# Kernel optimization log

Measured on AMD Instinct MI355X. Metric: run time of the kernel, lower is better.

Reference implementation:

```python
import jax, jax.numpy as jnp
import numpy as np

DIM = 240; NH = 6; HD = 20          # dim, num_heads, head_dim = dim // (2*num_heads)
WS = 16; BWS = 8                    # window size, base window size
R = (WS // BWS) ** 2                # spatial_linear in_features (=4)
LW = WS * WS; LB = BWS * BWS

# static relative-position index for a WSxWS window (same construction as torch buffer)
_coords = np.stack(np.meshgrid(np.arange(WS), np.arange(WS), indexing='ij')).reshape(2, -1)
_rel = (_coords[:, :, None] - _coords[:, None, :]).transpose(1, 2, 0).astype(np.int64)
_rel[..., 0] += WS - 1; _rel[..., 1] += WS - 1; _rel[..., 0] *= 2 * WS - 1
RPI = jnp.asarray(_rel.sum(-1))     # [LW, LW]


def conv2d(x, w, b, pad):
    y = jax.lax.conv_general_dilated(x, w, (1, 1), [(pad, pad), (pad, pad)],
                                     dimension_numbers=('NCHW', 'OIHW', 'NCHW'))
    return y + b[None, :, None, None]


def lrelu(x):
    return jnp.where(x >= 0, x, 0.2 * x)  # LeakyReLU(0.2)


def layer_norm(x, g, b, eps=1e-5):
    m = x.mean(-1, keepdims=True)
    v = jnp.mean((x - m) ** 2, axis=-1, keepdims=True)
    return (x - m) * jax.lax.rsqrt(v + eps) * g + b


def setup_inputs() -> dict:
    key = jax.random.key(0)
    ks = iter(jax.random.split(key, 40))
    rn = lambda shape: jax.random.normal(next(ks), shape, jnp.float32) * 0.02
    B, H, W = 2, 256, 256
    pd = (DIM // 4) // 4  # DynamicPosBias pos_dim = 15
    return {
        'x': jax.random.normal(next(ks), (B, H * W, DIM), jnp.float32),
        # DFE (qv projection)
        'c1_w': rn((DIM // 5, DIM, 1, 1)), 'c1_b': jnp.zeros((DIM // 5,), jnp.float32),
        'c2_w': rn((DIM // 5, DIM // 5, 3, 3)), 'c2_b': jnp.zeros((DIM // 5,), jnp.float32),
        'c3_w': rn((DIM, DIM // 5, 1, 1)), 'c3_b': jnp.zeros((DIM,), jnp.float32),
        'lin_w': rn((DIM, DIM, 1, 1)), 'lin_b': jnp.zeros((DIM,), jnp.float32),
        # spatial linear projection Linear(R, 1)
        'sl_w': rn((1, R)), 'sl_b': jnp.zeros((1,), jnp.float32),
        # DynamicPosBias MLP (residual=False)
        'pp_w': rn((pd, 2)), 'pp_b': jnp.zeros((pd,), jnp.float32),
        'ln1_g': jnp.ones((pd,), jnp.float32), 'ln1_b': jnp.zeros((pd,), jnp.float32),
        'p1_w': rn((pd, pd)), 'p1_b': jnp.zeros((pd,), jnp.float32),
        'ln2_g': jnp.ones((pd,), jnp.float32), 'ln2_b': jnp.zeros((pd,), jnp.float32),
        'p2_w': rn((pd, pd)), 'p2_b': jnp.zeros((pd,), jnp.float32),
        'ln3_g': jnp.ones((pd,), jnp.float32), 'ln3_b': jnp.zeros((pd,), jnp.float32),
        'p3_w': rn((NH, pd)), 'p3_b': jnp.zeros((NH,), jnp.float32),
        # output projection
        'proj_w': rn((DIM, DIM)), 'proj_b': jnp.zeros((DIM,), jnp.float32),
        'H': 256, 'W': 256,
    }


def reference(x, c1_w, c1_b, c2_w, c2_b, c3_w, c3_b, lin_w, lin_b, sl_w, sl_b,
              pp_w, pp_b, ln1_g, ln1_b, p1_w, p1_b, ln2_g, ln2_b, p2_w, p2_b,
              ln3_g, ln3_b, p3_w, p3_b, proj_w, proj_b, H, W):
    B, L, C = x.shape
    # ---- DFE feature projection (conv-gated) ----
    xi = jnp.transpose(x, (0, 2, 1)).reshape(B, C, H, W)
    conv = conv2d(lrelu(conv2d(lrelu(conv2d(xi, c1_w, c1_b, 0)), c2_w, c2_b, 1)), c3_w, c3_b, 0)
    qv = conv * conv2d(xi, lin_w, lin_b, 0)                       # [B,C,H,W]
    qv = jnp.transpose(qv, (0, 2, 3, 1))                          # [B,H,W,C]
    # ---- window partition ----
    nh_w, nw_w = H // WS, W // WS
    qv = qv.reshape(B, nh_w, WS, nw_w, WS, C).transpose(0, 1, 3, 2, 4, 5).reshape(-1, LW, C)
    B_ = qv.shape[0]
    qv = qv.reshape(B_, LW, 2, NH, HD).transpose(2, 0, 3, 1, 4)   # [2,B_,NH,LW,HD]
    q, v = qv[0], qv[1]
    # ---- spatial self-correlation ----
    # spatial linear projection of v: [B_,NH,LW,HD] -> [B_,NH,LB,HD]
    vs = v.reshape(B_, NH, BWS, WS // BWS, BWS, WS // BWS, HD)
    vs = vs.transpose(0, 1, 2, 4, 6, 3, 5).reshape(B_, NH, LB, HD, R)
    vs = jnp.einsum('bnkcr,or->bnkc', vs, sl_w) + sl_b            # Linear(R,1), squeezed
    corr = jnp.einsum('bnlc,bnkc->bnlk', q, vs) / HD              # [B_,NH,LW,LB]
    # dynamic relative position bias (MLP over the mother set of relative coords)
    ph = jnp.arange(1 - WS, WS)
    biases = jnp.stack(jnp.meshgrid(ph, ph, indexing='ij')).reshape(2, -1).T.astype(x.dtype)
    pos = biases @ pp_w.T + pp_b
    pos = jax.nn.relu(layer_norm(pos, ln1_g, ln1_b)) @ p1_w.T + p1_b
    pos = jax.nn.relu(layer_norm(pos, ln2_g, ln2_b)) @ p2_w.T + p2_b
    pos = jax.nn.relu(layer_norm(pos, ln3_g, ln3_b)) @ p3_w.T + p3_b  # [(2*WS-1)^2, NH]
    rpb = jnp.take(pos, RPI.reshape(-1), axis=0).reshape(LW, LW, NH).transpose(2, 0, 1)
    # pool key axis to base-window resolution (consistent with spatial_linear_projection grouping)
    rpb = rpb.reshape(NH, LW, BWS, WS // BWS, BWS, WS // BWS).mean((3, 5)).reshape(NH, LW, LB)
    corr = corr + rpb[None]
    x_s = jnp.einsum('bnlk,bnkc->bnlc', corr, vs)
    x_s = x_s.transpose(0, 2, 1, 3).reshape(B_, LW, NH * HD)      # [B_,LW,C/2]
    # ---- channel self-correlation (single-head over merged channels) ----
    qc = q.transpose(0, 2, 1, 3).reshape(B_, LW, NH * HD)
    vc = v.transpose(0, 2, 1, 3).reshape(B_, LW, NH * HD)
    corr_c = jnp.einsum('blc,bld->bcd', qc, vc) / LW              # [B_,C/2,C/2]
    x_c = jnp.einsum('bcd,bld->blc', corr_c, vc)                  # [B_,LW,C/2]
    # ---- window reverse + spatial-channel fusion ----
    def wrev(t):
        return t.reshape(B, nh_w, nw_w, WS, WS, -1).transpose(0, 1, 3, 2, 4, 5).reshape(B, H, W, -1)
    out = jnp.concatenate([wrev(x_s), wrev(x_c)], axis=-1)        # [B,H,W,C]
    out = out @ proj_w.T + proj_b
    return out.reshape(B, L, C)
```

## Files before the change

### kernel.cpp

```cpp
#include <hip/hip_runtime.h>
#include <math.h>

#define NPIX 131072

typedef __attribute__((ext_vector_type(8))) short bfrag;
typedef __attribute__((ext_vector_type(4))) float facc;
typedef __attribute__((ext_vector_type(4))) unsigned short us4;

__device__ __forceinline__ float lrelu_f(float x) { return x >= 0.f ? x : 0.2f * x; }

__device__ __forceinline__ int pix_of(int w, int l) {
    int b = w >> 8, wi = (w >> 4) & 15, wj = w & 15;
    return ((((b << 4) + wi) * 16 + (l >> 4)) << 8) + (wj << 4) + (l & 15);
}

__device__ __forceinline__ unsigned short bf16rn(float f) {
    unsigned u = __builtin_bit_cast(unsigned, f);
    u += 0x7FFFu + ((u >> 16) & 1u);
    return (unsigned short)(u >> 16);
}
__device__ __forceinline__ float bf16tof(unsigned short h) {
    unsigned u = ((unsigned)h) << 16;
    return __builtin_bit_cast(float, u);
}

__device__ __forceinline__ void split_x_body(const float* __restrict__ x,
                                             unsigned short* __restrict__ xs2, int idx)
{
    int row = idx >> 5;
    int k = (idx & 31) * 8;
    float v[8];
    if (k < 240) {
        float4 a = *(const float4*)(x + (size_t)row * 240 + k);
        float4 b = *(const float4*)(x + (size_t)row * 240 + k + 4);
        v[0] = a.x; v[1] = a.y; v[2] = a.z; v[3] = a.w;
        v[4] = b.x; v[5] = b.y; v[6] = b.z; v[7] = b.w;
    } else {
#pragma unroll
        for (int e = 0; e < 8; ++e) v[e] = 0.f;
    }
    bfrag hi, lo;
#pragma unroll
    for (int e = 0; e < 8; ++e) {
        unsigned short h = bf16rn(v[e]);
        hi[e] = (short)h;
        lo[e] = (short)bf16rn(v[e] - bf16tof(h));
    }
    unsigned short* dst = xs2 + (size_t)row * 512 + k;
    *(bfrag*)(dst) = hi;
    *(bfrag*)(dst + 256) = lo;
}

__device__ __forceinline__ void pack_w_body(const float* __restrict__ src,
                                            int rows, int K,
                                            unsigned short* __restrict__ dst,
                                            int total8, int KPAD, int idx)
{
    if (idx >= total8) return;
    int kper = KPAD >> 3;
    int row = idx / kper;
    int k = (idx - row * kper) * 8;
    float v[8];
#pragma unroll
    for (int e = 0; e < 8; ++e) {
        int kk = k + e;
        v[e] = (row < rows && kk < K) ? src[(size_t)row * K + kk] : 0.f;
    }
    bfrag hi, lo;
#pragma unroll
    for (int e = 0; e < 8; ++e) {
        unsigned short h = bf16rn(v[e]);
        hi[e] = (short)h;
        lo[e] = (short)bf16rn(v[e] - bf16tof(h));
    }
    unsigned short* d = dst + (size_t)row * 2 * KPAD + k;
    *(bfrag*)(d) = hi;
    *(bfrag*)(d + KPAD) = lo;
}

__device__ __forceinline__ void pack_c2w_body(const float* __restrict__ c2_w,
                                              unsigned short* __restrict__ c2w2, int idx)
{
    if (idx >= 6912) return;
    int rowid = idx >> 4;
    int c = idx & 15;
    int tap = rowid / 48, n = rowid - tap * 48;
    int ty = tap / 3, tx = tap - ty * 3;
    int lohalf = c >> 3;
    int cbase = (c & 7) * 8;
    bfrag outv;
#pragma unroll
    for (int e = 0; e < 8; ++e) {
        int ci = cbase + e;
        float v = (ci < 48) ? c2_w[(((size_t)n * 48 + ci) * 3 + ty) * 3 + tx] : 0.f;
        unsigned short h = bf16rn(v);
        outv[e] = (short)(lohalf ? bf16rn(v - bf16tof(h)) : h);
    }
    *(bfrag*)(c2w2 + (size_t)rowid * 128 + c * 8) = outv;
}

__global__ __launch_bounds__(256) void pack_all_kernel(
    const float* __restrict__ lin_w, const float* __restrict__ proj_w,
    const float* __restrict__ c3_w, const float* __restrict__ c1_w,
    const float* __restrict__ c2_w, const float* __restrict__ x,
    unsigned short* __restrict__ lin_w2, unsigned short* __restrict__ proj_w2,
    unsigned short* __restrict__ c3_w2, unsigned short* __restrict__ c1_w2,
    unsigned short* __restrict__ c2w2, unsigned short* __restrict__ xs2)
{
    int blk = blockIdx.x, tid = threadIdx.x;
    if (blk < 32)       pack_w_body(lin_w, 240, 240, lin_w2, 8192, 256, blk * 256 + tid);
    else if (blk < 64)  pack_w_body(proj_w, 240, 240, proj_w2, 8192, 256, (blk - 32) * 256 + tid);
    else if (blk < 72)  pack_w_body(c3_w, 240, 48, c3_w2, 2048, 64, (blk - 64) * 256 + tid);
    else if (blk < 88)  pack_w_body(c1_w, 48, 240, c1_w2, 4096, 256, (blk - 72) * 256 + tid);
    else if (blk < 115) pack_c2w_body(c2_w, c2w2, (blk - 88) * 256 + tid);
    else                split_x_body(x, xs2, (blk - 115) * 256 + tid);
}

__device__ __forceinline__ void ln_relu15(const float* h, float* r,
                                          const float* __restrict__ g,
                                          const float* __restrict__ b) {
    float m = 0.f;
#pragma unroll
    for (int f = 0; f < 15; ++f) m += h[f];
    m *= (1.f / 15.f);
    float v = 0.f;
#pragma unroll
    for (int f = 0; f < 15; ++f) { float d = h[f] - m; v += d * d; }
    float rs = rsqrtf(v * (1.f / 15.f) + 1e-5f);
#pragma unroll
    for (int f = 0; f < 15; ++f) {
        float xx = (h[f] - m) * rs * g[f] + b[f];
        r[f] = xx > 0.f ? xx : 0.f;
    }
}

__device__ __forceinline__ void lin15(const float* r, float* h,
                                      const float* __restrict__ w,
                                      const float* __restrict__ b) {
#pragma unroll
    for (int o = 0; o < 15; ++o) {
        float s = b[o];
#pragma unroll
        for (int g = 0; g < 15; ++g) s += r[g] * w[o * 15 + g];
        h[o] = s;
    }
}

__global__ __launch_bounds__(256) void prep_pos_kernel(
    const float* __restrict__ pp_w, const float* __restrict__ pp_b,
    const float* __restrict__ ln1_g, const float* __restrict__ ln1_b,
    const float* __restrict__ p1_w, const float* __restrict__ p1_b,
    const float* __restrict__ ln2_g, const float* __restrict__ ln2_b,
    const float* __restrict__ p2_w, const float* __restrict__ p2_b,
    const float* __restrict__ ln3_g, const float* __restrict__ ln3_b,
    const float* __restrict__ p3_w, const float* __restrict__ p3_b,
    float* __restrict__ pos3)
{
    int idx = blockIdx.x * 256 + threadIdx.x;
    if (idx >= 961) return;
    float h[15], r[15];
    float in0 = (float)(idx / 31) - 15.f;
    float in1 = (float)(idx % 31) - 15.f;
#pragma unroll
    for (int f = 0; f < 15; ++f) h[f] = in0 * pp_w[2 * f] + in1 * pp_w[2 * f + 1] + pp_b[f];
    ln_relu15(h, r, ln1_g, ln1_b);
    lin15(r, h, p1_w, p1_b);
    ln_relu15(h, r, ln2_g, ln2_b);
    lin15(r, h, p2_w, p2_b);
    ln_relu15(h, r, ln3_g, ln3_b);
#pragma unroll
    for (int o = 0; o < 6; ++o) {
        float s = p3_b[o];
#pragma unroll
        for (int g = 0; g < 15; ++g) s += r[g] * p3_w[o * 15 + g];
        pos3[idx * 6 + o] = s;
    }
}

__global__ __launch_bounds__(256) void rpb_kernel(const float* __restrict__ pos3,
                                                  float* __restrict__ rpb_t)
{
    int out = blockIdx.x * 256 + threadIdx.x;
    int n = out >> 14;
    int k = (out >> 8) & 63;
    int l = out & 255;
    int a = k >> 3, c = k & 7;
    int i1 = l >> 4, j1 = l & 15;
    float s = 0.f;
#pragma unroll
    for (int bb = 0; bb < 2; ++bb)
#pragma unroll
        for (int d = 0; d < 2; ++d) {
            int i2 = a * 2 + bb, j2 = c * 2 + d;
            int rpi = (i1 - i2 + 15) * 31 + (j1 - j2 + 15);
            s += pos3[rpi * 6 + n];
        }
    rpb_t[out] = s * 0.25f;
}

__device__ __forceinline__ void mfma_kpass3(const unsigned short* __restrict__ A2, int lda2,
                                            const unsigned short* __restrict__ W2, int ldw2,
                                            int ksteps, int mbase, int nbase,
                                            short* lds_a, short* lds_w,
                                            int tid, int wm, int wn,
                                            facc acc[4][4])
{
    int lane = tid & 63;
    int i = lane & 15, g = lane >> 4;
    int kpa = lda2 >> 1, kpw = ldw2 >> 1;
    for (int s = 0; s < ksteps; ++s) {
        int k0 = s * 32;
        {
            int r = tid >> 1, h16 = (tid & 1) * 16;
            const unsigned short* src = A2 + (size_t)(mbase + r) * lda2 + k0 + h16;
            bfrag h0 = *(const bfrag*)(src);
            bfrag h1 = *(const bfrag*)(src + 8);
            bfrag l0 = *(const bfrag*)(src + kpa);
            bfrag l1 = *(const bfrag*)(src + kpa + 8);
            short* dst = lds_a + r * 72 + h16;
            *(bfrag*)(dst)      = h0;  *(bfrag*)(dst + 8)  = h1;
            *(bfrag*)(dst + 32) = l0;  *(bfrag*)(dst + 40) = l1;
        }
        {
            int r = tid >> 1, half = tid & 1;
            const unsigned short* src = W2 + (size_t)(nbase + r) * ldw2 + half * kpw + k0;
            bfrag v0 = *(const bfrag*)(src);
            bfrag v1 = *(const bfrag*)(src + 8);
            bfrag v2 = *(const bfrag*)(src + 16);
            bfrag v3 = *(const bfrag*)(src + 24);
            short* dst = lds_w + r * 72 + half * 32;
            *(bfrag*)(dst)      = v0;  *(bfrag*)(dst + 8)  = v1;
            *(bfrag*)(dst + 16) = v2;  *(bfrag*)(dst + 24) = v3;
        }
        __syncthreads();
        bfrag ah[4], al[4], bh[4], bl[4];
#pragma unroll
        for (int mu = 0; mu < 4; ++mu) {
            const short* p = lds_a + (wm * 64 + mu * 16 + i) * 72 + g * 8;
            ah[mu] = *(const bfrag*)(p);
            al[mu] = *(const bfrag*)(p + 32);
        }
#pragma unroll
        for (int nu = 0; nu < 4; ++nu) {
            const short* p = lds_w + (wn * 64 + nu * 16 + i) * 72 + g * 8;
            bh[nu] = *(const bfrag*)(p);
            bl[nu] = *(const bfrag*)(p + 32);
        }
#pragma unroll
        for (int mu = 0; mu < 4; ++mu)
#pragma unroll
            for (int nu = 0; nu < 4; ++nu) {
                acc[mu][nu] = __builtin_amdgcn_mfma_f32_16x16x32_bf16(ah[mu], bh[nu], acc[mu][nu], 0, 0, 0);
                acc[mu][nu] = __builtin_amdgcn_mfma_f32_16x16x32_bf16(ah[mu], bl[nu], acc[mu][nu], 0, 0, 0);
                acc[mu][nu] = __builtin_amdgcn_mfma_f32_16x16x32_bf16(al[mu], bh[nu], acc[mu][nu], 0, 0, 0);
            }
        __syncthreads();
    }
}

__device__ __forceinline__ void mfma_kpass_n64(const unsigned short* __restrict__ A2, int lda2,
                                               const unsigned short* __restrict__ W2, int ldw2,
                                               int ksteps, int mbase,
                                               short* lds_a, short* lds_w,
                                               int tid, int wm, int wn,
                                               facc acc[4][2])
{
    int lane = tid & 63;
    int i = lane & 15, g = lane >> 4;
    int kpa = lda2 >> 1, kpw = ldw2 >> 1;
    for (int s = 0; s < ksteps; ++s) {
        int k0 = s * 32;
        {
            int r = tid >> 1, h16 = (tid & 1) * 16;
            const unsigned short* src = A2 + (size_t)(mbase + r) * lda2 + k0 + h16;
            bfrag h0 = *(const bfrag*)(src);
            bfrag h1 = *(const bfrag*)(src + 8);
            bfrag l0 = *(const bfrag*)(src + kpa);
            bfrag l1 = *(const bfrag*)(src + kpa + 8);
            short* dst = lds_a + r * 72 + h16;
            *(bfrag*)(dst)      = h0;  *(bfrag*)(dst + 8)  = h1;
            *(bfrag*)(dst + 32) = l0;  *(bfrag*)(dst + 40) = l1;
        }
        if (tid < 128) {
            int r = tid >> 1, half = tid & 1;
            const unsigned short* src = W2 + (size_t)r * ldw2 + half * kpw + k0;
            bfrag v0 = *(const bfrag*)(src);
            bfrag v1 = *(const bfrag*)(src + 8);
            bfrag v2 = *(const bfrag*)(src + 16);
            bfrag v3 = *(const bfrag*)(src + 24);
            short* dst = lds_w + r * 72 + half * 32;
            *(bfrag*)(dst)      = v0;  *(bfrag*)(dst + 8)  = v1;
            *(bfrag*)(dst + 16) = v2;  *(bfrag*)(dst + 24) = v3;
        }
        __syncthreads();
        bfrag ah[4], al[4], bh[2], bl[2];
#pragma unroll
        for (int mu = 0; mu < 4; ++mu) {
            const short* p = lds_a + (wm * 64 + mu * 16 + i) * 72 + g * 8;
            ah[mu] = *(const bfrag*)(p);
            al[mu] = *(const bfrag*)(p + 32);
        }
#pragma unroll
        for (int nu = 0; nu < 2; ++nu) {
            const short* p = lds_w + (wn * 32 + nu * 16 + i) * 72 + g * 8;
            bh[nu] = *(const bfrag*)(p);
            bl[nu] = *(const bfrag*)(p + 32);
        }
#pragma unroll
        for (int mu = 0; mu < 4; ++mu)
#pragma unroll
            for (int nu = 0; nu < 2; ++nu) {
                acc[mu][nu] = __builtin_amdgcn_mfma_f32_16x16x32_bf16(ah[mu], bh[nu], acc[mu][nu], 0, 0, 0);
                acc[mu][nu] = __builtin_amdgcn_mfma_f32_16x16x32_bf16(ah[mu], bl[nu], acc[mu][nu], 0, 0, 0);
                acc[mu][nu] = __builtin_amdgcn_mfma_f32_16x16x32_bf16(al[mu], bh[nu], acc[mu][nu], 0, 0, 0);
            }
        __syncthreads();
    }
}

__global__ __launch_bounds__(256, 3) void conv1_mfma_kernel(const unsigned short* __restrict__ xs2,
    const unsigned short* __restrict__ c1_w2, const float* __restrict__ bias,
    unsigned short* __restrict__ t1s)
{
    __shared__ __align__(16) short lds_a[128 * 72];
    __shared__ __align__(16) short lds_w[64 * 72];
    int tid = threadIdx.x;
    int lane = tid & 63, wid = tid >> 6;
    int wm = wid >> 1, wn = wid & 1;
    int mbase = blockIdx.x * 128;
    facc zero = {0.f, 0.f, 0.f, 0.f};
    facc acc[4][2];
#pragma unroll
    for (int mu = 0; mu < 4; ++mu)
#pragma unroll
        for (int nu = 0; nu < 2; ++nu) acc[mu][nu] = zero;

    mfma_kpass_n64(xs2, 512, c1_w2, 512, 8, mbase, lds_a, lds_w, tid, wm, wn, acc);

    int i = lane & 15, g = lane >> 4;
#pragma unroll
    for (int nu = 0; nu < 2; ++nu) {
        int n = wn * 32 + nu * 16 + i;
        if (n < 48) {
            float bv = bias[n];
#pragma unroll
            for (int mu = 0; mu < 4; ++mu)
#pragma unroll
                for (int rr = 0; rr < 4; ++rr) {
                    size_t m = (size_t)mbase + wm * 64 + mu * 16 + g * 4 + rr;
                    float v = lrelu_f(acc[mu][nu][rr] + bv);
                    unsigned short h = bf16rn(v);
                    t1s[m * 128 + n] = h;
                    t1s[m * 128 + 64 + n] = bf16rn(v - bf16tof(h));
                }
        }
    }
    if (tid < 128) {
        size_t m = (size_t)mbase + tid;
        bfrag z = {0, 0, 0, 0, 0, 0, 0, 0};
        *(bfrag*)(t1s + m * 128 + 48)  = z;
        *(bfrag*)(t1s + m * 128 + 56)  = z;
        *(bfrag*)(t1s + m * 128 + 112) = z;
        *(bfrag*)(t1s + m * 128 + 120) = z;
    }
}

__global__ __launch_bounds__(256) void conv2_mfma_kernel(const unsigned short* __restrict__ t1s,
    const unsigned short* __restrict__ c2w2, const float* __restrict__ bias,
    unsigned short* __restrict__ t2s)
{
    __shared__ __align__(16) short a_s[130 * 128];
    int bid = blockIdx.x;
    int xcd = bid & 7;
    int j = bid >> 3;
    int half = j & 1;
    int rl = (j >> 1) & 31;
    int b = j >> 6;
    int r = xcd * 32 + rl;
    int c0 = half * 128;
    int tid = threadIdx.x;
    int lane = tid & 63, wid = tid >> 6;
    int i = lane & 15, g = lane >> 4;
    facc zero = {0.f, 0.f, 0.f, 0.f};
    facc acc[2][3];
#pragma unroll
    for (int mu = 0; mu < 2; ++mu)
#pragma unroll
        for (int nu = 0; nu < 3; ++nu) acc[mu][nu] = zero;

    for (int dy = 0; dy < 3; ++dy) {
        int grow = r + dy - 1;
        bool rowok = (grow >= 0 && grow < 256);
        for (int idx = tid; idx < 130 * 16; idx += 256) {
            int j2 = idx >> 4, ch = idx & 15;
            int gc = c0 - 1 + j2;
            bfrag v = {0, 0, 0, 0, 0, 0, 0, 0};
            if (rowok && gc >= 0 && gc < 256) {
                size_t gpix = ((size_t)b * 256 + grow) * 256 + gc;
                v = *(const bfrag*)(t1s + gpix * 128 + ch * 8);
            }
            *(bfrag*)&a_s[j2 * 128 + ((ch ^ (j2 & 7)) * 8)] = v;
        }
        __syncthreads();
#pragma unroll
        for (int dx = 0; dx < 3; ++dx) {
            const unsigned short* wb = c2w2 + (size_t)(dy * 3 + dx) * 48 * 128;
#pragma unroll
            for (int h = 0; h < 2; ++h) {
                bfrag ah[2], al[2], bh[3], bl[3];
#pragma unroll
                for (int mu = 0; mu < 2; ++mu) {
                    int j2 = wid * 32 + mu * 16 + i + dx;
                    int chi = (h * 4 + g) ^ (j2 & 7);
                    int clo = (8 + h * 4 + g) ^ (j2 & 7);
                    ah[mu] = *(const bfrag*)&a_s[j2 * 128 + chi * 8];
                    al[mu] = *(const bfrag*)&a_s[j2 * 128 + clo * 8];
                }
#pragma unroll
                for (int nu = 0; nu < 3; ++nu) {
                    const unsigned short* wp = wb + (size_t)(nu * 16 + i) * 128 + h * 32 + g * 8;
                    bh[nu] = *(const bfrag*)(wp);
                    bl[nu] = *(const bfrag*)(wp + 64);
                }
#pragma unroll
                for (int mu = 0; mu < 2; ++mu)
#pragma unroll
                    for (int nu = 0; nu < 3; ++nu) {
                        acc[mu][nu] = __builtin_amdgcn_mfma_f32_16x16x32_bf16(ah[mu], bh[nu], acc[mu][nu], 0, 0, 0);
                        acc[mu][nu] = __builtin_amdgcn_mfma_f32_16x16x32_bf16(ah[mu], bl[nu], acc[mu][nu], 0, 0, 0);
                        acc[mu][nu] = __builtin_amdgcn_mfma_f32_16x16x32_bf16(al[mu], bh[nu], acc[mu][nu], 0, 0, 0);
                    }
            }
        }
        __syncthreads();
    }
#pragma unroll
    for (int nu = 0; nu < 3; ++nu) {
        int n = nu * 16 + i;
        float bv = bias[n];
#pragma unroll
        for (int mu = 0; mu < 2; ++mu)
#pragma unroll
            for (int rr = 0; rr < 4; ++rr) {
                int lp = wid * 32 + mu * 16 + g * 4 + rr;
                size_t gpix = ((size_t)b * 256 + r) * 256 + (c0 + lp);
                float v = lrelu_f(acc[mu][nu][rr] + bv);
                unsigned short h = bf16rn(v);
                t2s[gpix * 128 + n] = h;
                t2s[gpix * 128 + 64 + n] = bf16rn(v - bf16tof(h));
            }
    }
    if (tid < 128) {
        size_t gpix = ((size_t)b * 256 + r) * 256 + (c0 + tid);
        bfrag z = {0, 0, 0, 0, 0, 0, 0, 0};
        *(bfrag*)(t2s + gpix * 128 + 48)  = z;
        *(bfrag*)(t2s + gpix * 128 + 56)  = z;
        *(bfrag*)(t2s + gpix * 128 + 112) = z;
        *(bfrag*)(t2s + gpix * 128 + 120) = z;
    }
}

__global__ __launch_bounds__(256) void qv_mfma_kernel(const unsigned short* __restrict__ xs2,
    const unsigned short* __restrict__ lin_w2, const float* __restrict__ lin_b,
    const unsigned short* __restrict__ t2s, const unsigned short* __restrict__ c3_w2,
    const float* __restrict__ c3_b, float* __restrict__ qv)
{
    __shared__ __align__(16) short lds_a[128 * 72];
    __shared__ __align__(16) short lds_w[128 * 72];
    int tid = threadIdx.x;
    int lane = tid & 63, wid = tid >> 6;
    int wm = wid >> 1, wn = wid & 1;
    int bid = blockIdx.y * 2 + blockIdx.x;
    int xcd = bid & 7, j = bid >> 3;
    int mbase = (xcd * 128 + (j >> 1)) * 128;
    int nbase = (j & 1) * 128;
    facc zero = {0.f, 0.f, 0.f, 0.f};
    facc acc1[4][4], acc2[4][4];
#pragma unroll
    for (int mu = 0; mu < 4; ++mu)
#pragma unroll
        for (int nu = 0; nu < 4; ++nu) { acc1[mu][nu] = zero; acc2[mu][nu] = zero; }

    mfma_kpass3(xs2, 512, lin_w2, 512, 8, mbase, nbase, lds_a, lds_w, tid, wm, wn, acc1);
    mfma_kpass3(t2s, 128, c3_w2, 128, 2, mbase, nbase, lds_a, lds_w, tid, wm, wn, acc2);

    int i = lane & 15, g = lane >> 4;
#pragma unroll
    for (int nu = 0; nu < 4; ++nu) {
        int n = nbase + wn * 64 + nu * 16 + i;
        if (n < 240) {
            float lb = lin_b[n], cb = c3_b[n];
#pragma unroll
            for (int mu = 0; mu < 4; ++mu)
#pragma unroll
                for (int rr = 0; rr < 4; ++rr) {
                    size_t m = (size_t)mbase + wm * 64 + mu * 16 + g * 4 + rr;
                    qv[m * 240 + n] = (acc2[mu][nu][rr] + cb) * (acc1[mu][nu][rr] + lb);
                }
        }
    }
}

__global__ __launch_bounds__(256, 3) void proj_mfma_kernel(const unsigned short* __restrict__ cat2,
    const unsigned short* __restrict__ proj_w2, const float* __restrict__ bias,
    float* __restrict__ out)
{
    __shared__ __align__(16) short lds_a[128 * 72];
    __shared__ __align__(16) short lds_w[128 * 72];
    int tid = threadIdx.x;
    int lane = tid & 63, wid = tid >> 6;
    int wm = wid >> 1, wn = wid & 1;
    int bid = blockIdx.y * 2 + blockIdx.x;
    int xcd = bid & 7, j = bid >> 3;
    int mbase = (xcd * 128 + (j >> 1)) * 128;
    int nbase = (j & 1) * 128;
    facc zero = {0.f, 0.f, 0.f, 0.f};
    facc acc[4][4];
#pragma unroll
    for (int mu = 0; mu < 4; ++mu)
#pragma unroll
        for (int nu = 0; nu < 4; ++nu) acc[mu][nu] = zero;

    mfma_kpass3(cat2, 512, proj_w2, 512, 8, mbase, nbase, lds_a, lds_w, tid, wm, wn, acc);

    int i = lane & 15, g = lane >> 4;
#pragma unroll
    for (int nu = 0; nu < 4; ++nu) {
        int n = nbase + wn * 64 + nu * 16 + i;
        if (n < 240) {
            float bv = bias[n];
#pragma unroll
            for (int mu = 0; mu < 4; ++mu)
#pragma unroll
                for (int rr = 0; rr < 4; ++rr) {
                    size_t m = (size_t)mbase + wm * 64 + mu * 16 + g * 4 + rr;
                    out[m * 240 + n] = acc[mu][nu][rr] + bv;
                }
        }
    }
}

__global__ __launch_bounds__(256) void xs_kernel(const float* __restrict__ qv,
    const float* __restrict__ rpb_t, const float* __restrict__ sl_w,
    const float* __restrict__ sl_b, unsigned short* __restrict__ cat2)
{
    __shared__ __align__(16) float v_s[256 * 20];
    __shared__ __align__(16) float vs_s[64 * 20];
    int bid = blockIdx.x;
    int xcd = bid & 7;
    int j = bid >> 3;
    int wl = j / 6;
    int n = j - wl * 6;
    int w = xcd * 64 + wl;
    int tid = threadIdx.x;
    int l = tid;
    size_t pix = (size_t)pix_of(w, l);
    const float* qp = qv + pix * 240 + n * 20;
    float qr[20];
#pragma unroll
    for (int h4 = 0; h4 < 5; ++h4) {
        *(float4*)&qr[h4 * 4] = *(const float4*)(qp + h4 * 4);
        *(float4*)&v_s[l * 20 + h4 * 4] = *(const float4*)(qp + 120 + h4 * 4);
    }
    __syncthreads();
    float slw0 = sl_w[0], slw1 = sl_w[1], slw2 = sl_w[2], slw3 = sl_w[3];
    float slb = sl_b[0];
    for (int idx = tid; idx < 1280; idx += 256) {
        int k = idx / 20, hd = idx % 20;
        int a = k >> 3, c = k & 7;
        int l00 = a * 32 + c * 2;
        float vsum = slb
                   + slw0 * v_s[(l00 + 0) * 20 + hd]
                   + slw1 * v_s[(l00 + 1) * 20 + hd]
                   + slw2 * v_s[(l00 + 16) * 20 + hd]
                   + slw3 * v_s[(l00 + 17) * 20 + hd];
        vs_s[idx] = vsum;
    }
    __syncthreads();
    const float* rp = rpb_t + (size_t)n * 16384 + l;
    float acc[20];
#pragma unroll
    for (int hd = 0; hd < 20; ++hd) acc[hd] = 0.f;
#pragma unroll
    for (int k = 0; k < 64; ++k) {
        float vr[20];
#pragma unroll
        for (int h4 = 0; h4 < 5; ++h4)
            *(float4*)&vr[h4 * 4] = *(const float4*)&vs_s[k * 20 + h4 * 4];
        float s0 = 0.f, s1 = 0.f, s2 = 0.f, s3 = 0.f;
#pragma unroll
        for (int hd = 0; hd < 20; hd += 4) {
            s0 += qr[hd + 0] * vr[hd + 0];
            s1 += qr[hd + 1] * vr[hd + 1];
            s2 += qr[hd + 2] * vr[hd + 2];
            s3 += qr[hd + 3] * vr[hd + 3];
        }
        float cc = (s0 + s1 + s2 + s3) * (1.f / 20.f) + rp[(size_t)k * 256];
#pragma unroll
        for (int hd = 0; hd < 20; ++hd) acc[hd] += cc * vr[hd];
    }
    unsigned short* op = cat2 + pix * 512 + n * 20;
#pragma unroll
    for (int h4 = 0; h4 < 5; ++h4) {
        us4 h, lo;
#pragma unroll
        for (int e = 0; e < 4; ++e) {
            float v = acc[h4 * 4 + e];
            unsigned short hh = bf16rn(v);
            h[e] = hh;
            lo[e] = bf16rn(v - bf16tof(hh));
        }
        *(us4*)(op + h4 * 4) = h;
        *(us4*)(op + 256 + h4 * 4) = lo;
    }
    if (n == 0) {
        bfrag z = {0, 0, 0, 0, 0, 0, 0, 0};
        unsigned short* zp = cat2 + pix * 512;
        *(bfrag*)(zp + 240) = z;  *(bfrag*)(zp + 248) = z;
        *(bfrag*)(zp + 496) = z;  *(bfrag*)(zp + 504) = z;
    }
}

__global__ __launch_bounds__(256) void corrxc_kernel(const float* __restrict__ qv,
                                                     unsigned short* __restrict__ cat2)
{
    extern __shared__ short smem[];
    short* lds_g = smem;
    short* ph1_a = smem;
    short* ph1_w = smem + 9216;
    short* ph2_a = smem + 33792;

    int bid = blockIdx.x;
    int w = (bid & 7) * 64 + (bid >> 3);
    int tid = threadIdx.x;
    int lane = tid & 63, wid = tid >> 6;
    int wm = wid >> 1, wn = wid & 1;
    int i = lane & 15, g = lane >> 4;
    facc zero = {0.f, 0.f, 0.f, 0.f};
    facc acc[4][4];
#pragma unroll
    for (int mu = 0; mu < 4; ++mu)
#pragma unroll
        for (int nu = 0; nu < 4; ++nu) acc[mu][nu] = zero;

    for (int l0 = 0; l0 < 256; l0 += 32) {
        int dl = tid & 31;
        int ch0 = (tid >> 5) * 16;
        const float* qp = qv + (size_t)pix_of(w, l0 + dl) * 240;
#pragma unroll
        for (int j4 = 0; j4 < 4; ++j4) {
            int c0 = ch0 + j4 * 4;
            float4 fa = make_float4(0.f, 0.f, 0.f, 0.f);
            float4 fb = make_float4(0.f, 0.f, 0.f, 0.f);
            if (c0 < 120) {
                fa = *(const float4*)(qp + 120 + c0);
                fb = *(const float4*)(qp + c0);
            }
            float ea[4] = {fa.x, fa.y, fa.z, fa.w};
            float eb[4] = {fb.x, fb.y, fb.z, fb.w};
#pragma unroll
            for (int e = 0; e < 4; ++e) {
                int ch = c0 + e;
                unsigned short h = bf16rn(ea[e]);
                ph1_a[ch * 72 + dl]      = (short)h;
                ph1_a[ch * 72 + 32 + dl] = (short)bf16rn(ea[e] - bf16tof(h));
                h = bf16rn(eb[e]);
                ph1_w[ch * 72 + dl]      = (short)h;
                ph1_w[ch * 72 + 32 + dl] = (short)bf16rn(eb[e] - bf16tof(h));
            }
        }
        __syncthreads();
        bfrag ah[4], al2[4], bh[4], bl2[4];
#pragma unroll
        for (int mu = 0; mu < 4; ++mu) {
            const short* p = ph1_a + (wm * 64 + mu * 16 + i) * 72 + g * 8;
            ah[mu] = *(const bfrag*)(p);
            al2[mu] = *(const bfrag*)(p + 32);
        }
#pragma unroll
        for (int nu = 0; nu < 4; ++nu) {
            const short* p = ph1_w + (wn * 64 + nu * 16 + i) * 72 + g * 8;
            bh[nu] = *(const bfrag*)(p);
            bl2[nu] = *(const bfrag*)(p + 32);
        }
#pragma unroll
        for (int mu = 0; mu < 4; ++mu)
#pragma unroll
            for (int nu = 0; nu < 4; ++nu) {
                acc[mu][nu] = __builtin_amdgcn_mfma_f32_16x16x32_bf16(ah[mu], bh[nu], acc[mu][nu], 0, 0, 0);
                acc[mu][nu] = __builtin_amdgcn_mfma_f32_16x16x32_bf16(ah[mu], bl2[nu], acc[mu][nu], 0, 0, 0);
                acc[mu][nu] = __builtin_amdgcn_mfma_f32_16x16x32_bf16(al2[mu], bh[nu], acc[mu][nu], 0, 0, 0);
            }
        __syncthreads();
    }
#pragma unroll
    for (int mu = 0; mu < 4; ++mu)
#pragma unroll
        for (int nu = 0; nu < 4; ++nu)
#pragma unroll
            for (int rr = 0; rr < 4; ++rr) {
                int d = wm * 64 + mu * 16 + g * 4 + rr;
                int c = wn * 64 + nu * 16 + i;
                float v = acc[mu][nu][rr];
                unsigned short h = bf16rn(v);
                lds_g[c * 264 + d]       = (short)h;
                lds_g[c * 264 + 128 + d] = (short)bf16rn(v - bf16tof(h));
            }

    for (int mh = 0; mh < 2; ++mh) {
#pragma unroll
        for (int mu = 0; mu < 4; ++mu)
#pragma unroll
            for (int nu = 0; nu < 4; ++nu) acc[mu][nu] = zero;
        for (int k0 = 0; k0 < 128; k0 += 32) {
            {
                int r = tid >> 1, h16 = (tid & 1) * 16;
                const float* qp = qv + (size_t)pix_of(w, mh * 128 + r) * 240 + 120;
                float v[16];
#pragma unroll
                for (int j4 = 0; j4 < 4; ++j4) {
                    int d0 = k0 + h16 + j4 * 4;
                    float4 f = make_float4(0.f, 0.f, 0.f, 0.f);
                    if (d0 < 120) f = *(const float4*)(qp + d0);
                    v[j4 * 4 + 0] = f.x; v[j4 * 4 + 1] = f.y;
                    v[j4 * 4 + 2] = f.z; v[j4 * 4 + 3] = f.w;
                }
                bfrag h0, h1, lo0, lo1;
#pragma unroll
                for (int e = 0; e < 8; ++e) {
                    unsigned short h = bf16rn(v[e]);
                    h0[e] = (short)h;
                    lo0[e] = (short)bf16rn(v[e] - bf16tof(h));
                    h = bf16rn(v[8 + e]);
                    h1[e] = (short)h;
                    lo1[e] = (short)bf16rn(v[8 + e] - bf16tof(h));
                }
                short* dst = ph2_a + r * 72 + h16;
                *(bfrag*)(dst)      = h0;  *(bfrag*)(dst + 8)  = h1;
                *(bfrag*)(dst + 32) = lo0; *(bfrag*)(dst + 40) = lo1;
            }
            __syncthreads();
            bfrag ah[4], al2[4], bh[4], bl2[4];
#pragma unroll
            for (int mu = 0; mu < 4; ++mu) {
                const short* p = ph2_a + (wm * 64 + mu * 16 + i) * 72 + g * 8;
                ah[mu] = *(const bfrag*)(p);
                al2[mu] = *(const bfrag*)(p + 32);
            }
#pragma unroll
            for (int nu = 0; nu < 4; ++nu) {
                const short* p = lds_g + (wn * 64 + nu * 16 + i) * 264 + k0 + g * 8;
                bh[nu] = *(const bfrag*)(p);
                bl2[nu] = *(const bfrag*)(p + 128);
            }
#pragma unroll
            for (int mu = 0; mu < 4; ++mu)
#pragma unroll
                for (int nu = 0; nu < 4; ++nu) {
                    acc[mu][nu] = __builtin_amdgcn_mfma_f32_16x16x32_bf16(ah[mu], bh[nu], acc[mu][nu], 0, 0, 0);
                    acc[mu][nu] = __builtin_amdgcn_mfma_f32_16x16x32_bf16(ah[mu], bl2[nu], acc[mu][nu], 0, 0, 0);
                    acc[mu][nu] = __builtin_amdgcn_mfma_f32_16x16x32_bf16(al2[mu], bh[nu], acc[mu][nu], 0, 0, 0);
                }
            __syncthreads();
        }
#pragma unroll
        for (int mu = 0; mu < 4; ++mu) {
#pragma unroll
            for (int rr = 0; rr < 4; ++rr) {
                int l = mh * 128 + wm * 64 + mu * 16 + g * 4 + rr;
                size_t pix = (size_t)pix_of(w, l);
                unsigned short* op = cat2 + pix * 512;
#pragma unroll
                for (int nu = 0; nu < 4; ++nu) {
                    int c = wn * 64 + nu * 16 + i;
                    if (c < 120) {
                        float v = acc[mu][nu][rr] * (1.f / 256.f);
                        unsigned short h = bf16rn(v);
                        op[120 + c] = h;
                        op[256 + 120 + c] = bf16rn(v - bf16tof(h));
                    }
                }
            }
        }
    }
}

extern "C" void kernel_launch(void* const* d_in, const int* in_sizes, int n_in,
                              void* d_out, int out_size, void* d_ws, size_t ws_size,
                              hipStream_t stream)
{
    (void)in_sizes; (void)n_in; (void)out_size;
    const float* x     = (const float*)d_in[0];
    const float* c1_w  = (const float*)d_in[1];
    const float* c1_b  = (const float*)d_in[2];
    const float* c2_w  = (const float*)d_in[3];
    const float* c2_b  = (const float*)d_in[4];
    const float* c3_w  = (const float*)d_in[5];
    const float* c3_b  = (const float*)d_in[6];
    const float* lin_w = (const float*)d_in[7];
    const float* lin_b = (const float*)d_in[8];
    const float* sl_w  = (const float*)d_in[9];
    const float* sl_b  = (const float*)d_in[10];
    const float* pp_w  = (const float*)d_in[11];
    const float* pp_b  = (const float*)d_in[12];
    const float* ln1_g = (const float*)d_in[13];
    const float* ln1_b = (const float*)d_in[14];
    const float* p1_w  = (const float*)d_in[15];
    const float* p1_b  = (const float*)d_in[16];
    const float* ln2_g = (const float*)d_in[17];
    const float* ln2_b = (const float*)d_in[18];
    const float* p2_w  = (const float*)d_in[19];
    const float* p2_b  = (const float*)d_in[20];
    const float* ln3_g = (const float*)d_in[21];
    const float* ln3_b = (const float*)d_in[22];
    const float* p3_w  = (const float*)d_in[23];
    const float* p3_b  = (const float*)d_in[24];
    const float* proj_w = (const float*)d_in[25];
    const float* proj_b = (const float*)d_in[26];

    float* ws = (float*)d_ws;
    float* pos3   = ws;
    float* rpb_t  = ws + 8192;
    unsigned short* lin_w2  = (unsigned short*)(ws + 106496);
    unsigned short* c3_w2   = (unsigned short*)(ws + 172032);
    unsigned short* proj_w2 = (unsigned short*)(ws + 188416);
    unsigned short* c1_w2   = (unsigned short*)(ws + 253952);
    unsigned short* c2w2    = (unsigned short*)(ws + 286720);
    unsigned short* t2s = (unsigned short*)(ws + 314368);
    unsigned short* xs2 = (unsigned short*)(ws + 8702976);
    unsigned short* cat2 = xs2;
    float* qvb    = ws + 42257408;
    unsigned short* t1s = (unsigned short*)qvb;
    const size_t required = (size_t)73714688 * 4;
    if (ws_size < required) return;

    pack_all_kernel<<<16499, 256, 0, stream>>>(lin_w, proj_w, c3_w, c1_w, c2_w, x,
                                               lin_w2, proj_w2, c3_w2, c1_w2, c2w2, xs2);
    prep_pos_kernel<<<4, 256, 0, stream>>>(pp_w, pp_b, ln1_g, ln1_b, p1_w, p1_b,
                                           ln2_g, ln2_b, p2_w, p2_b, ln3_g, ln3_b,
                                           p3_w, p3_b, pos3);
    rpb_kernel<<<384, 256, 0, stream>>>(pos3, rpb_t);
    conv1_mfma_kernel<<<1024, 256, 0, stream>>>(xs2, c1_w2, c1_b, t1s);
    conv2_mfma_kernel<<<1024, 256, 0, stream>>>(t1s, c2w2, c2_b, t2s);
    qv_mfma_kernel<<<dim3(2, 1024), 256, 0, stream>>>(xs2, lin_w2, lin_b, t2s, c3_w2, c3_b, qvb);
    xs_kernel<<<3072, 256, 0, stream>>>(qvb, rpb_t, sl_w, sl_b, cat2);
    corrxc_kernel<<<512, 256, 86016, stream>>>(qvb, cat2);
    proj_mfma_kernel<<<dim3(2, 1024), 256, 0, stream>>>(cat2, proj_w2, proj_b, (float*)d_out);
}
```

Measured before the change: 508.8 us.

## Rewrite spatial correlation kernel to use split-bf16 MFMA for both matmuls

The per-window spatial correlation (q·vs then corr·vs) moves from per-thread scalar FP32 FMA loops onto MFMA 16x16x32 bf16 instructions. Near-FP32 accuracy is kept with a hi/lo bf16 split and three MFMAs per product. Operands are staged in LDS, the correlation matrix plus bias round-trips through LDS between the two GEMMs, and the block now requests about 80KB of dynamic shared memory. In exchange there are many more syncs and conversions, scattered 2-byte global stores, and lower occupancy from the larger LDS footprint.

```diff
diff --git a/kernel.cpp b/kernel.cpp
--- a/kernel.cpp
+++ b/kernel.cpp
@@ -540,12 +540,18 @@
     }
 }
 
-__global__ __launch_bounds__(256) void xs_kernel(const float* __restrict__ qv,
+__global__ __launch_bounds__(256) void xs_mfma_kernel(const float* __restrict__ qv,
     const float* __restrict__ rpb_t, const float* __restrict__ sl_w,
     const float* __restrict__ sl_b, unsigned short* __restrict__ cat2)
 {
-    __shared__ __align__(16) float v_s[256 * 20];
-    __shared__ __align__(16) float vs_s[64 * 20];
+    extern __shared__ short smem[];
+    short* qs    = smem;
+    float* v_s   = (float*)(smem + 18432);
+    float* vs_s  = (float*)(smem + 28672);
+    short* vsW   = smem + 31232;
+    short* vsT   = smem + 35840;
+    short* corrS = smem;
+
     int bid = blockIdx.x;
     int xcd = bid & 7;
     int j = bid >> 3;
@@ -553,67 +559,169 @@
     int n = j - wl * 6;
     int w = xcd * 64 + wl;
     int tid = threadIdx.x;
-    int l = tid;
-    size_t pix = (size_t)pix_of(w, l);
-    const float* qp = qv + pix * 240 + n * 20;
-    float qr[20];
-#pragma unroll
-    for (int h4 = 0; h4 < 5; ++h4) {
-        *(float4*)&qr[h4 * 4] = *(const float4*)(qp + h4 * 4);
-        *(float4*)&v_s[l * 20 + h4 * 4] = *(const float4*)(qp + 120 + h4 * 4);
+    int lane = tid & 63, wv = tid >> 6;
+    int i = lane & 15, gg = lane >> 4;
+
+    {
+        int l = tid;
+        size_t pix = (size_t)pix_of(w, l);
+        const float* qp = qv + pix * 240 + n * 20;
+        unsigned short hi[32], lo[32];
+#pragma unroll
+        for (int hd = 0; hd < 20; ++hd) {
+            float v = qp[hd];
+            unsigned short h = bf16rn(v);
+            hi[hd] = h;
+            lo[hd] = bf16rn(v - bf16tof(h));
+        }
+#pragma unroll
+        for (int hd = 20; hd < 32; ++hd) { hi[hd] = 0; lo[hd] = 0; }
+        short* dst = qs + l * 72;
+#pragma unroll
+        for (int c8 = 0; c8 < 4; ++c8) {
+            *(bfrag*)(dst + c8 * 8)      = *(const bfrag*)&hi[c8 * 8];
+            *(bfrag*)(dst + 32 + c8 * 8) = *(const bfrag*)&lo[c8 * 8];
+        }
+#pragma unroll
+        for (int h4 = 0; h4 < 5; ++h4)
+            *(float4*)&v_s[l * 20 + h4 * 4] = *(const float4*)(qp + 120 + h4 * 4);
     }
     __syncthreads();
-    float slw0 = sl_w[0], slw1 = sl_w[1], slw2 = sl_w[2], slw3 = sl_w[3];
-    float slb = sl_b[0];
-    for (int idx = tid; idx < 1280; idx += 256) {
-        int k = idx / 20, hd = idx % 20;
-        int a = k >> 3, c = k & 7;
-        int l00 = a * 32 + c * 2;
-        float vsum = slb
-                   + slw0 * v_s[(l00 + 0) * 20 + hd]
-                   + slw1 * v_s[(l00 + 1) * 20 + hd]
-                   + slw2 * v_s[(l00 + 16) * 20 + hd]
-                   + slw3 * v_s[(l00 + 17) * 20 + hd];
-        vs_s[idx] = vsum;
+    {
+        float slw0 = sl_w[0], slw1 = sl_w[1], slw2 = sl_w[2], slw3 = sl_w[3];
+        float slb = sl_b[0];
+        for (int idx = tid; idx < 1280; idx += 256) {
+            int k = idx / 20, hd = idx % 20;
+            int a = k >> 3, c = k & 7;
+            int l00 = a * 32 + c * 2;
+            vs_s[idx] = slb
+                      + slw0 * v_s[(l00 + 0) * 20 + hd]
+                      + slw1 * v_s[(l00 + 1) * 20 + hd]
+                      + slw2 * v_s[(l00 + 16) * 20 + hd]
+                      + slw3 * v_s[(l00 + 17) * 20 + hd];
+        }
     }
     __syncthreads();
-    const float* rp = rpb_t + (size_t)n * 16384 + l;
-    float acc[20];
-#pragma unroll
-    for (int hd = 0; hd < 20; ++hd) acc[hd] = 0.f;
-#pragma unroll
-    for (int k = 0; k < 64; ++k) {
-        float vr[20];
-#pragma unroll
-        for (int h4 = 0; h4 < 5; ++h4)
-            *(float4*)&vr[h4 * 4] = *(const float4*)&vs_s[k * 20 + h4 * 4];
-        float s0 = 0.f, s1 = 0.f, s2 = 0.f, s3 = 0.f;
-#pragma unroll
-        for (int hd = 0; hd < 20; hd += 4) {
-            s0 += qr[hd + 0] * vr[hd + 0];
-            s1 += qr[hd + 1] * vr[hd + 1];
-            s2 += qr[hd + 2] * vr[hd + 2];
-            s3 += qr[hd + 3] * vr[hd + 3];
-        }
-        float cc = (s0 + s1 + s2 + s3) * (1.f / 20.f) + rp[(size_t)k * 256];
-#pragma unroll
-        for (int hd = 0; hd < 20; ++hd) acc[hd] += cc * vr[hd];
-    }
-    unsigned short* op = cat2 + pix * 512 + n * 20;
-#pragma unroll
-    for (int h4 = 0; h4 < 5; ++h4) {
-        us4 h, lo;
-#pragma unroll
-        for (int e = 0; e < 4; ++e) {
-            float v = acc[h4 * 4 + e];
-            unsigned short hh = bf16rn(v);
-            h[e] = hh;
-            lo[e] = bf16rn(v - bf16tof(hh));
-        }
-        *(us4*)(op + h4 * 4) = h;
-        *(us4*)(op + 256 + h4 * 4) = lo;
+    {
+        int k = tid >> 2, q4 = tid & 3;
+        int hd0 = q4 * 8;
+        unsigned short hi[8], lo[8];
+#pragma unroll
+        for (int e = 0; e < 8; ++e) {
+            int hd = hd0 + e;
+            float v = (hd < 20) ? vs_s[k * 20 + hd] : 0.f;
+            unsigned short h = bf16rn(v);
+            hi[e] = h;
+            lo[e] = bf16rn(v - bf16tof(h));
+        }
+        *(bfrag*)(vsW + k * 72 + hd0)      = *(const bfrag*)hi;
+        *(bfrag*)(vsW + k * 72 + 32 + hd0) = *(const bfrag*)lo;
+        for (int idx = tid; idx < 2048; idx += 256) {
+            int hd = idx >> 6, kk = idx & 63;
+            float v = (hd < 20) ? vs_s[kk * 20 + hd] : 0.f;
+            unsigned short h = bf16rn(v);
+            vsT[hd * 136 + kk]      = (short)h;
+            vsT[hd * 136 + 64 + kk] = (short)bf16rn(v - bf16tof(h));
+        }
+    }
+    __syncthreads();
+    facc zero = {0.f, 0.f, 0.f, 0.f};
+    facc acc[4][4];
+#pragma unroll
+    for (int mu = 0; mu < 4; ++mu)
+#pragma unroll
+        for (int nu = 0; nu < 4; ++nu) acc[mu][nu] = zero;
+    {
+        bfrag ah[4], al[4], bh[4], bl[4];
+#pragma unroll
+        for (int mu = 0; mu < 4; ++mu) {
+            const short* p = qs + (wv * 64 + mu * 16 + i) * 72 + gg * 8;
+            ah[mu] = *(const bfrag*)(p);
+            al[mu] = *(const bfrag*)(p + 32);
+        }
+#pragma unroll
+        for (int nu = 0; nu < 4; ++nu) {
+            const short* p = vsW + (nu * 16 + i) * 72 + gg * 8;
+            bh[nu] = *(const bfrag*)(p);
+            bl[nu] = *(const bfrag*)(p + 32);
+        }
+#pragma unroll
+        for (int mu = 0; mu < 4; ++mu)
+#pragma unroll
+            for (int nu = 0; nu < 4; ++nu) {
+                acc[mu][nu] = __builtin_amdgcn_mfma_f32_16x16x32_bf16(ah[mu], bh[nu], acc[mu][nu], 0, 0, 0);
+                acc[mu][nu] = __builtin_amdgcn_mfma_f32_16x16x32_bf16(ah[mu], bl[nu], acc[mu][nu], 0, 0, 0);
+                acc[mu][nu] = __builtin_amdgcn_mfma_f32_16x16x32_bf16(al[mu], bh[nu], acc[mu][nu], 0, 0, 0);
+            }
+    }
+    __syncthreads();
+    {
+        const float* rp = rpb_t + (size_t)n * 16384;
+#pragma unroll
+        for (int mu = 0; mu < 4; ++mu)
+#pragma unroll
+            for (int nu = 0; nu < 4; ++nu)
+#pragma unroll
+                for (int rr = 0; rr < 4; ++rr) {
+                    int l = wv * 64 + mu * 16 + gg * 4 + rr;
+                    int k = nu * 16 + i;
+                    float c = acc[mu][nu][rr] * (1.f / 20.f) + rp[(size_t)k * 256 + l];
+                    unsigned short h = bf16rn(c);
+                    corrS[l * 136 + k]      = (short)h;
+                    corrS[l * 136 + 64 + k] = (short)bf16rn(c - bf16tof(h));
+                }
+    }
+    __syncthreads();
+    facc acc2[4][2];
+#pragma unroll
+    for (int mu = 0; mu < 4; ++mu)
+#pragma unroll
+        for (int nu = 0; nu < 2; ++nu) acc2[mu][nu] = zero;
+#pragma unroll
+    for (int ks = 0; ks < 2; ++ks) {
+        int k0 = ks * 32;
+        bfrag ah[4], al[4], bh[2], bl[2];
+#pragma unroll
+        for (int mu = 0; mu < 4; ++mu) {
+            const short* p = corrS + (wv * 64 + mu * 16 + i) * 136 + k0 + gg * 8;
+            ah[mu] = *(const bfrag*)(p);
+            al[mu] = *(const bfrag*)(p + 64);
+        }
+#pragma unroll
+        for (int nu = 0; nu < 2; ++nu) {
+            const short* p = vsT + (nu * 16 + i) * 136 + k0 + gg * 8;
+            bh[nu] = *(const bfrag*)(p);
+            bl[nu] = *(const bfrag*)(p + 64);
+        }
+#pragma unroll
+        for (int mu = 0; mu < 4; ++mu)
+#pragma unroll
+            for (int nu = 0; nu < 2; ++nu) {
+                acc2[mu][nu] = __builtin_amdgcn_mfma_f32_16x16x32_bf16(ah[mu], bh[nu], acc2[mu][nu], 0, 0, 0);
+                acc2[mu][nu] = __builtin_amdgcn_mfma_f32_16x16x32_bf16(ah[mu], bl[nu], acc2[mu][nu], 0, 0, 0);
+                acc2[mu][nu] = __builtin_amdgcn_mfma_f32_16x16x32_bf16(al[mu], bh[nu], acc2[mu][nu], 0, 0, 0);
+            }
+    }
+#pragma unroll
+    for (int nu = 0; nu < 2; ++nu) {
+        int hd = nu * 16 + i;
+        if (hd < 20) {
+#pragma unroll
+            for (int mu = 0; mu < 4; ++mu)
+#pragma unroll
+                for (int rr = 0; rr < 4; ++rr) {
+                    int l = wv * 64 + mu * 16 + gg * 4 + rr;
+                    size_t pix = (size_t)pix_of(w, l);
+                    unsigned short* op = cat2 + pix * 512;
+                    float v = acc2[mu][nu][rr];
+                    unsigned short h = bf16rn(v);
+                    op[n * 20 + hd] = h;
+                    op[256 + n * 20 + hd] = bf16rn(v - bf16tof(h));
+                }
+        }
     }
     if (n == 0) {
+        size_t pix = (size_t)pix_of(w, tid);
         bfrag z = {0, 0, 0, 0, 0, 0, 0, 0};
         unsigned short* zp = cat2 + pix * 512;
         *(bfrag*)(zp + 240) = z;  *(bfrag*)(zp + 248) = z;
@@ -843,7 +951,7 @@
     conv1_mfma_kernel<<<1024, 256, 0, stream>>>(xs2, c1_w2, c1_b, t1s);
     conv2_mfma_kernel<<<1024, 256, 0, stream>>>(t1s, c2w2, c2_b, t2s);
     qv_mfma_kernel<<<dim3(2, 1024), 256, 0, stream>>>(xs2, lin_w2, lin_b, t2s, c3_w2, c3_b, qvb);
-    xs_kernel<<<3072, 256, 0, stream>>>(qvb, rpb_t, sl_w, sl_b, cat2);
+    xs_mfma_kernel<<<3072, 256, 80384, stream>>>(qvb, rpb_t, sl_w, sl_b, cat2);
     corrxc_kernel<<<512, 256, 86016, stream>>>(qvb, cat2);
     proj_mfma_kernel<<<dim3(2, 1024), 256, 0, stream>>>(cat2, proj_w2, proj_b, (float*)d_out);
 }
```

Result: no change. 507.9 us (-0.2%).
